# Optimization experiments

Measured on AMD Instinct MI355X. Metric: run time of the kernel, lower is better.

Reference implementation:

```python
import jax, jax.numpy as jnp
import numpy as np

D_MODEL = 1024
D_INNER = 2048   # expand * d_model
D_STATE = 16
D_CONV = 4
DT_RANK = 64     # ceil(d_model / 16)
BATCH = 4
SEQLEN = 2048


def _dw_causal_conv(x, w, b):
    # x: (B, d, L); w: (d, 1, K) depthwise; causal left pad K-1 -> output length L
    y = jax.lax.conv_general_dilated(
        x, w, window_strides=(1,), padding=[(D_CONV - 1, 0)],
        dimension_numbers=("NCH", "OIH", "NCH"), feature_group_count=x.shape[1])
    return y + b[None, :, None]


def _ssm_pass(x_conv, z, A_log, x_proj_w, dt_proj_w, dt_proj_b, D):
    # x_conv, z: (B, d, L)
    Bsz, d, L = x_conv.shape
    u = jax.nn.silu(x_conv)                                   # (B, d, L)
    x_dbl = jnp.einsum("bdl,rd->blr", u, x_proj_w)            # (B, L, dt_rank+2N)
    dt = x_dbl[..., :DT_RANK]
    Bm = x_dbl[..., DT_RANK:DT_RANK + D_STATE]                # (B, L, N)
    Cm = x_dbl[..., DT_RANK + D_STATE:]                       # (B, L, N)
    delta = jax.nn.softplus(jnp.einsum("blr,dr->bld", dt, dt_proj_w) + dt_proj_b)  # (B, L, d)
    A = -jnp.exp(A_log)                                       # (d, N)

    # time-major inputs for scan
    delta_t = jnp.transpose(delta, (1, 0, 2))                 # (L, B, d)
    u_t = jnp.transpose(u, (2, 0, 1))                         # (L, B, d)
    Bm_t = jnp.transpose(Bm, (1, 0, 2))                       # (L, B, N)
    Cm_t = jnp.transpose(Cm, (1, 0, 2))                       # (L, B, N)

    def step(h, inp):
        d_s, B_s, C_s, u_s = inp                              # (B,d) (B,N) (B,N) (B,d)
        dA = jnp.exp(d_s[:, :, None] * A)                     # (B, d, N)
        h = dA * h + (d_s * u_s)[:, :, None] * B_s[:, None, :]
        y = jnp.einsum("bdn,bn->bd", h, C_s)
        return h, y

    h0 = jnp.zeros((Bsz, d, D_STATE), dtype=u.dtype)
    _, ys = jax.lax.scan(step, h0, (delta_t, Bm_t, Cm_t, u_t))  # ys: (L, B, d)
    y = jnp.transpose(ys, (1, 2, 0)) + D[None, :, None] * u     # (B, d, L)
    return y * jax.nn.silu(z)


def setup_inputs() -> dict:
    key = jax.random.key(0)
    ks = jax.random.split(key, 16)
    s = 0.02
    hidden_states = jax.random.normal(ks[0], (BATCH, SEQLEN, D_MODEL), jnp.float32)
    in_proj_w = jax.random.normal(ks[1], (2 * D_INNER, D_MODEL), jnp.float32) * s
    conv_w_f = jax.random.normal(ks[2], (D_INNER, 1, D_CONV), jnp.float32) * 0.2
    conv_b_f = jax.random.normal(ks[3], (D_INNER,), jnp.float32) * 0.1
    conv_w_b = jax.random.normal(ks[4], (D_INNER, 1, D_CONV), jnp.float32) * 0.2
    conv_b_b = jax.random.normal(ks[5], (D_INNER,), jnp.float32) * 0.1
    x_proj_w_f = jax.random.normal(ks[6], (DT_RANK + 2 * D_STATE, D_INNER), jnp.float32) * s
    dt_proj_w_f = jax.random.uniform(ks[7], (D_INNER, DT_RANK), jnp.float32, -DT_RANK**-0.5, DT_RANK**-0.5)
    x_proj_w_b = jax.random.normal(ks[8], (DT_RANK + 2 * D_STATE, D_INNER), jnp.float32) * s
    dt_proj_w_b = jax.random.uniform(ks[9], (D_INNER, DT_RANK), jnp.float32, -DT_RANK**-0.5, DT_RANK**-0.5)
    # dt bias init: inverse-softplus of dt sampled log-uniform in [1e-3, 1e-1]
    dt = jnp.exp(jax.random.uniform(ks[10], (D_INNER,)) * (np.log(0.1) - np.log(0.001)) + np.log(0.001))
    dt = jnp.clip(dt, 1e-4, None)
    inv_dt = dt + jnp.log(-jnp.expm1(-dt))
    dt_proj_b_f = inv_dt
    dt_proj_b_b = inv_dt
    A_log = jnp.log(jnp.broadcast_to(jnp.arange(1, D_STATE + 1, dtype=jnp.float32), (D_INNER, D_STATE)))
    out_proj_w = jax.random.normal(ks[11], (D_MODEL, D_INNER), jnp.float32) * s
    return {
        "hidden_states": hidden_states, "in_proj_w": in_proj_w,
        "conv_w_f": conv_w_f, "conv_b_f": conv_b_f, "conv_w_b": conv_w_b, "conv_b_b": conv_b_b,
        "x_proj_w_f": x_proj_w_f, "dt_proj_w_f": dt_proj_w_f, "dt_proj_b_f": dt_proj_b_f,
        "x_proj_w_b": x_proj_w_b, "dt_proj_w_b": dt_proj_w_b, "dt_proj_b_b": dt_proj_b_b,
        "A_log_f": A_log, "A_log_b": A_log,
        "D_f": jnp.ones((D_INNER,), jnp.float32), "D_b": jnp.ones((D_INNER,), jnp.float32),
        "out_proj_w": out_proj_w,
    }


def reference(hidden_states, in_proj_w, conv_w_f, conv_b_f, conv_w_b, conv_b_b,
              x_proj_w_f, dt_proj_w_f, dt_proj_b_f, x_proj_w_b, dt_proj_w_b, dt_proj_b_b,
              A_log_f, A_log_b, D_f, D_b, out_proj_w):
    L = hidden_states.shape[1]
    xz = jnp.einsum("bld,ed->bel", hidden_states, in_proj_w)  # (B, 2*d_inner, L)
    x, z = xz[:, :D_INNER], xz[:, D_INNER:]

    # forward direction
    x_conv_f = _dw_causal_conv(x, conv_w_f, conv_b_f)[..., :L]
    y_f = _ssm_pass(x_conv_f, z, A_log_f, x_proj_w_f, dt_proj_w_f, dt_proj_b_f, D_f)

    # backward direction
    x_b, z_b = x[..., ::-1], z[..., ::-1]
    x_conv_b = _dw_causal_conv(x_b, conv_w_b, conv_b_b)[..., :L]
    y_b = _ssm_pass(x_conv_b, z_b, A_log_b, x_proj_w_b, dt_proj_w_b, dt_proj_b_b, D_b)[..., ::-1]

    y = (y_f + y_b) / 2.0                                     # if_divide_out=True
    out = jnp.einsum("bdl,ed->ble", y, out_proj_w)            # (B, L, d_model)
    return out
```

## Files before the change

kernel.cpp:

```cpp
#include <hip/hip_runtime.h>


#define Bsz  4
#define LSEQ 2048
#define DM   1024
#define DI   2048
#define DS   16
#define MROWS (Bsz * LSEQ)
#define NCH  32
#define CLEN 64

typedef unsigned short u16b;
typedef __attribute__((ext_vector_type(8))) short short8;
typedef __attribute__((ext_vector_type(4))) float f32x4;
typedef __attribute__((address_space(3))) unsigned int lds_u32;
typedef const __attribute__((address_space(1))) unsigned int glb_u32;

__device__ __forceinline__ float b2f(u16b u) {
  union { unsigned int i; float f; } x; x.i = ((unsigned int)u) << 16; return x.f;
}
__device__ __forceinline__ u16b f2b(float f) {
  union { float f; unsigned int i; } x; x.f = f;
  unsigned int r = x.i + 0x7FFFu + ((x.i >> 16) & 1u);
  return (u16b)(r >> 16);
}
__device__ __forceinline__ u16b f2b_cvt(float f) {
  unsigned int r;
  asm("v_cvt_pk_bf16_f32 %0, %1, %1" : "=v"(r) : "v"(f));
  return (u16b)r;
}
__device__ __forceinline__ float fast_rcp(float x) {
  return __builtin_amdgcn_rcpf(x);
}
__device__ __forceinline__ float softplus_fast(float v) {
  float e = __expf(-fabsf(v));
  return fmaxf(v, 0.f) + __logf(1.f + e);
}
__device__ __forceinline__ void pow_ladder(float q, float* dA) {
  float q2 = q * q, q3 = q2 * q, q4 = q2 * q2;
  float q5 = q4 * q, q6 = q4 * q2, q7 = q4 * q3, q8 = q4 * q4;
  dA[0] = q;  dA[1] = q2;  dA[2] = q3;  dA[3] = q4;
  dA[4] = q5; dA[5] = q6;  dA[6] = q7;  dA[7] = q8;
  dA[8] = q8 * q;  dA[9] = q8 * q2;  dA[10] = q8 * q3;  dA[11] = q8 * q4;
  dA[12] = q8 * q5; dA[13] = q8 * q6; dA[14] = q8 * q7; dA[15] = q8 * q8;
}

__device__ __forceinline__ int xcd_swz(int id, int nwg) {
  int c = nwg >> 3;
  return (id & 7) * c + (id >> 3);
}

__device__ __forceinline__ void stage_tile(const u16b* gbase, int ld,
                                           u16b* lds, int wave, int lane) {
#pragma unroll
  for (int t = 0; t < 4; ++t) {
    int rb = wave * 32 + t * 8;
    int r = rb + (lane >> 3);
    int cb = (lane & 7) ^ (r & 7);
    const u16b* g = gbase + (size_t)r * ld + cb * 8;
    __builtin_amdgcn_global_load_lds((glb_u32*)g, (lds_u32*)(lds + rb * 64),
                                     16, 0, 0);
  }
}

__device__ __forceinline__ void stage_half(const u16b* gbase, int ld,
                                           u16b* ldsbase, int tid) {
#pragma unroll
  for (int i2 = 0; i2 < 2; ++i2) {
    int rg = (tid >> 6) * 2 + i2;
    int row = rg * 8 + ((tid >> 3) & 7);
    int cb = (tid & 7) ^ (row & 7);
    const u16b* g = gbase + (size_t)row * ld + cb * 8;
    __builtin_amdgcn_global_load_lds((glb_u32*)g,
                                     (lds_u32*)(ldsbase + rg * 8 * 64), 16, 0, 0);
  }
}

__global__ void sniff_kernel(const unsigned int* __restrict__ p,
                             int* __restrict__ flag) {
  unsigned int w = p[threadIdx.x];
  int e = (w >> 7) & 0xFF;
  unsigned long long m = __ballot(e >= 110 && e <= 135);
  if (threadIdx.x == 0) *flag = (__popcll(m) >= 32) ? 1 : 0;
}

struct ConvTab { const void* s[17]; u16b* d[17]; };
__global__ __launch_bounds__(256) void convert_all_kernel(
    ConvTab t, const int* __restrict__ flag) {
  const int pref[18] = {0, 4096, 6144, 7168, 7172, 7173, 7177, 7178, 7274,
                        7338, 7339, 7435, 7499, 7500, 7516, 7532, 7533, 7534};
  int bx = blockIdx.x;
  int seg = 0;
#pragma unroll
  for (int i = 0; i < 17; ++i)
    if (bx >= pref[i + 1]) seg = i + 1;
  int idx = (bx - pref[seg]) * 2048 + threadIdx.x * 8;
  u16b* dst = t.d[seg];
  if (*flag) {
    *(uint4*)(dst + idx) = *(const uint4*)((const u16b*)t.s[seg] + idx);
  } else {
    const float* s = (const float*)t.s[seg];
    float4 a = *(const float4*)(s + idx);
    float4 b = *(const float4*)(s + idx + 4);
    u16b o[8] = {f2b(a.x), f2b(a.y), f2b(a.z), f2b(a.w),
                 f2b(b.x), f2b(b.y), f2b(b.z), f2b(b.w)};
    *(uint4*)(dst + idx) = *(uint4*)o;
  }
}

__global__ __launch_bounds__(512, 2) void gemm8_kernel(
    const u16b* __restrict__ A, const u16b* __restrict__ B,
    u16b* __restrict__ C, int M, int N, int K, int lda, int ldb, int ldc) {
  __shared__ u16b As[2][256 * 64];
  __shared__ u16b Bs[2][256 * 64];
  const int tid = threadIdx.x;
  const int nbx = gridDim.x;
  const int id = xcd_swz(blockIdx.y * nbx + blockIdx.x, nbx * gridDim.y);
  const int n0 = (id % nbx) * 256;
  const int m0 = (id / nbx) * 256;
  const int wave = tid >> 6, lane = tid & 63;
  const int wm = (wave >> 2) * 128, wn = (wave & 3) * 64;
  const int lr = lane & 15, lg = lane >> 4;

  const u16b* Ab = A + (size_t)m0 * lda;
  const u16b* Bb = B + (size_t)n0 * ldb;
  const int nt = K >> 6;

  f32x4 acc[8][4] = {};

  stage_half(Ab, lda, As[0], tid);
  stage_half(Ab + (size_t)128 * lda, lda, As[0] + 8192, tid);
  stage_half(Bb, ldb, Bs[0], tid);
  stage_half(Bb + (size_t)128 * ldb, ldb, Bs[0] + 8192, tid);
  asm volatile("s_waitcnt vmcnt(0)" ::: "memory");
  __builtin_amdgcn_s_barrier();

  for (int t = 0; t < nt; ++t) {
    const int cur = t & 1;
    const u16b* Ac = As[cur];
    const u16b* Bc = Bs[cur];
    u16b* An = As[cur ^ 1];
    u16b* Bn = Bs[cur ^ 1];
    const int k1 = (t + 1) << 6;
    const bool more = (t + 1 < nt);
#pragma unroll
    for (int q = 0; q < 4; ++q) {
      short8 afr[4][2], bfr[2][2];
#pragma unroll
      for (int i = 0; i < 4; ++i) {
        int r = wm + (q >> 1) * 64 + i * 16 + lr;
#pragma unroll
        for (int kx = 0; kx < 2; ++kx)
          afr[i][kx] = *(const short8*)&Ac[r * 64 + ((kx * 4 + lg) ^ (r & 7)) * 8];
      }
#pragma unroll
      for (int j = 0; j < 2; ++j) {
        int r = wn + (q & 1) * 32 + j * 16 + lr;
#pragma unroll
        for (int kx = 0; kx < 2; ++kx)
          bfr[j][kx] = *(const short8*)&Bc[r * 64 + ((kx * 4 + lg) ^ (r & 7)) * 8];
      }
      if (more) {
        if (q == 0) stage_half(Ab + k1, lda, An, tid);
        else if (q == 1) stage_half(Ab + (size_t)128 * lda + k1, lda, An + 8192, tid);
        else if (q == 2) stage_half(Bb + k1, ldb, Bn, tid);
        else stage_half(Bb + (size_t)128 * ldb + k1, ldb, Bn + 8192, tid);
      }
      __builtin_amdgcn_s_barrier();
      asm volatile("s_waitcnt lgkmcnt(0)" ::: "memory");
      __builtin_amdgcn_sched_barrier(0);
      __builtin_amdgcn_s_setprio(1);
#pragma unroll
      for (int kx = 0; kx < 2; ++kx)
#pragma unroll
        for (int i = 0; i < 4; ++i)
#pragma unroll
          for (int j = 0; j < 2; ++j)
            acc[(q >> 1) * 4 + i][(q & 1) * 2 + j] =
                __builtin_amdgcn_mfma_f32_16x16x32_bf16(
                    afr[i][kx], bfr[j][kx],
                    acc[(q >> 1) * 4 + i][(q & 1) * 2 + j], 0, 0, 0);
      __builtin_amdgcn_s_setprio(0);
      __builtin_amdgcn_sched_barrier(0);
      __builtin_amdgcn_s_barrier();
    }
    asm volatile("s_waitcnt vmcnt(0)" ::: "memory");
    __builtin_amdgcn_s_barrier();
  }

#pragma unroll
  for (int i = 0; i < 8; ++i) {
    int rbase = m0 + wm + i * 16 + lg * 4;
#pragma unroll
    for (int j = 0; j < 4; ++j) {
      int col = n0 + wn + j * 16 + lr;
      if (col < N) {
#pragma unroll
        for (int e = 0; e < 4; ++e)
          C[(size_t)(rbase + e) * ldc + col] = f2b(acc[i][j][e]);
      }
    }
  }
}

#define BM 128
#define BN 128
#define BK 64

template<int EPI>
__global__ __launch_bounds__(256) void gemm_kernel(
    const u16b* __restrict__ A, const u16b* __restrict__ B, void* __restrict__ Cptr,
    const int* __restrict__ flag, int M, int N, int K, int lda, int ldb, int ldc) {
  __shared__ u16b As[BM * BK];
  __shared__ u16b Bs[BN * BK];
  const int tid = threadIdx.x;
  const int nbx = gridDim.x;
  const int id = xcd_swz(blockIdx.y * nbx + blockIdx.x, nbx * gridDim.y);
  const int n0 = (id % nbx) * BN;
  const int m0 = (id / nbx) * BM;
  const int wave = tid >> 6, lane = tid & 63;
  const int wm = (wave >> 1) * 64, wn = (wave & 1) * 64;
  const int lr = lane & 15, lg = lane >> 4;
  u16b* C = (u16b*)Cptr;
  float* Cf = (float*)Cptr;
  const int fl = (EPI == 3) ? flag[0] : 1;

  f32x4 acc[4][4] = {};

  for (int k0 = 0; k0 < K; k0 += BK) {
    stage_tile(A + (size_t)m0 * lda + k0, lda, As, wave, lane);
    stage_tile(B + (size_t)n0 * ldb + k0, ldb, Bs, wave, lane);
    __syncthreads();
#pragma unroll
    for (int kk = 0; kk < BK; kk += 32) {
      short8 afr[4], bfr[4];
#pragma unroll
      for (int i = 0; i < 4; ++i) {
        int r = wm + i * 16 + lr;
        afr[i] = *(const short8*)&As[r * 64 + (((kk >> 3) + lg) ^ (r & 7)) * 8];
      }
#pragma unroll
      for (int j = 0; j < 4; ++j) {
        int r = wn + j * 16 + lr;
        bfr[j] = *(const short8*)&Bs[r * 64 + (((kk >> 3) + lg) ^ (r & 7)) * 8];
      }
#pragma unroll
      for (int i = 0; i < 4; ++i)
#pragma unroll
        for (int j = 0; j < 4; ++j)
          acc[i][j] = __builtin_amdgcn_mfma_f32_16x16x32_bf16(
              afr[i], bfr[j], acc[i][j], 0, 0, 0);
    }
    __syncthreads();
  }

#pragma unroll
  for (int i = 0; i < 4; ++i) {
    int rbase = m0 + wm + i * 16 + lg * 4;
#pragma unroll
    for (int j = 0; j < 4; ++j) {
      int col = n0 + wn + j * 16 + lr;
      if (col < N) {
#pragma unroll
        for (int e = 0; e < 4; ++e) {
          float v = acc[i][j][e];
          size_t ci = (size_t)(rbase + e) * ldc + col;
          if (EPI == 3) {
            if (fl) C[ci] = f2b(v); else Cf[ci] = v;
          } else {
            C[ci] = f2b(v);
          }
        }
      }
    }
  }
}

template<int EPI>
__global__ __launch_bounds__(256) void gemm2_kernel(
    const u16b* __restrict__ A, const u16b* __restrict__ B1,
    const u16b* __restrict__ B2, u16b* __restrict__ C1, u16b* __restrict__ C2,
    const u16b* __restrict__ bias1, const u16b* __restrict__ bias2,
    float* __restrict__ aux1, float* __restrict__ aux2,
    int Mhalf, int N, int K, int lda, int ldb, int ldc1, int ldc2) {
  __shared__ u16b As[BM * BK];
  __shared__ u16b Bs[BN * BK];
  const int tid = threadIdx.x;
  const int nbx = gridDim.x;
  const int id = xcd_swz(blockIdx.y * nbx + blockIdx.x, nbx * gridDim.y);
  const int n0 = (id % nbx) * BN;
  const int m0 = (id / nbx) * BM;
  const int hi = (m0 >= Mhalf);
  const u16b* B = hi ? B2 : B1;
  u16b* C = hi ? C2 : C1;
  const u16b* bias = hi ? bias2 : bias1;
  float* aux = hi ? aux2 : aux1;
  const int ldc = hi ? ldc2 : ldc1;
  const int mloc = m0 - (hi ? Mhalf : 0);
  const int wave = tid >> 6, lane = tid & 63;
  const int wm = (wave >> 1) * 64, wn = (wave & 1) * 64;
  const int lr = lane & 15, lg = lane >> 4;

  f32x4 acc[4][4] = {};

  for (int k0 = 0; k0 < K; k0 += BK) {
    stage_tile(A + (size_t)m0 * lda + k0, lda, As, wave, lane);
    stage_tile(B + (size_t)n0 * ldb + k0, ldb, Bs, wave, lane);
    __syncthreads();
#pragma unroll
    for (int kk = 0; kk < BK; kk += 32) {
      short8 afr[4], bfr[4];
#pragma unroll
      for (int i = 0; i < 4; ++i) {
        int r = wm + i * 16 + lr;
        afr[i] = *(const short8*)&As[r * 64 + (((kk >> 3) + lg) ^ (r & 7)) * 8];
      }
#pragma unroll
      for (int j = 0; j < 4; ++j) {
        int r = wn + j * 16 + lr;
        bfr[j] = *(const short8*)&Bs[r * 64 + (((kk >> 3) + lg) ^ (r & 7)) * 8];
      }
#pragma unroll
      for (int i = 0; i < 4; ++i)
#pragma unroll
        for (int j = 0; j < 4; ++j)
          acc[i][j] = __builtin_amdgcn_mfma_f32_16x16x32_bf16(
              afr[i], bfr[j], acc[i][j], 0, 0, 0);
    }
    __syncthreads();
  }

#pragma unroll
  for (int i = 0; i < 4; ++i) {
    int rbase = mloc + wm + i * 16 + lg * 4;
#pragma unroll
    for (int j = 0; j < 4; ++j) {
      int col = n0 + wn + j * 16 + lr;
      if (col < N) {
        float bv = (EPI == 1) ? b2f(bias[col]) : 0.f;
#pragma unroll
        for (int e = 0; e < 4; ++e) {
          float v = acc[i][j][e];
          if (EPI == 1) v = softplus_fast(v + bv);
          C[(size_t)(rbase + e) * ldc + col] = f2b(v);
          if (EPI == 2 && col >= 64)
            aux[(size_t)(rbase + e) * 32 + (col - 64)] = v;
        }
      }
    }
  }
}

__global__ __launch_bounds__(256) void gemm2s_kernel(
    const u16b* __restrict__ A, const u16b* __restrict__ B1,
    const u16b* __restrict__ B2, float* __restrict__ P,
    int Mhalf, int Ksplit, int lda, int ldb) {
  __shared__ u16b As[BM * BK];
  __shared__ u16b Bs[BN * BK];
  const int tid = threadIdx.x;
  const int ks = blockIdx.x;
  const int m0 = blockIdx.y * BM;
  const int hi = (m0 >= Mhalf);
  const u16b* B = hi ? B2 : B1;
  const int wave = tid >> 6, lane = tid & 63;
  const int wm = (wave >> 1) * 64, wn = (wave & 1) * 64;
  const int lr = lane & 15, lg = lane >> 4;

  f32x4 acc[4][4] = {};

  const int kbeg = ks * Ksplit;
  for (int k0 = kbeg; k0 < kbeg + Ksplit; k0 += BK) {
    stage_tile(A + (size_t)m0 * lda + k0, lda, As, wave, lane);
    stage_tile(B + k0, ldb, Bs, wave, lane);
    __syncthreads();
#pragma unroll
    for (int kk = 0; kk < BK; kk += 32) {
      short8 afr[4], bfr[4];
#pragma unroll
      for (int i = 0; i < 4; ++i) {
        int r = wm + i * 16 + lr;
        afr[i] = *(const short8*)&As[r * 64 + (((kk >> 3) + lg) ^ (r & 7)) * 8];
      }
#pragma unroll
      for (int j = 0; j < 4; ++j) {
        int r = wn + j * 16 + lr;
        bfr[j] = *(const short8*)&Bs[r * 64 + (((kk >> 3) + lg) ^ (r & 7)) * 8];
      }
#pragma unroll
      for (int i = 0; i < 4; ++i)
#pragma unroll
        for (int j = 0; j < 4; ++j)
          acc[i][j] = __builtin_amdgcn_mfma_f32_16x16x32_bf16(
              afr[i], bfr[j], acc[i][j], 0, 0, 0);
    }
    __syncthreads();
  }

  float* Pk = P + (size_t)ks * ((size_t)2 * Mhalf) * 128;
#pragma unroll
  for (int i = 0; i < 4; ++i) {
    int rg = m0 + wm + i * 16 + lg * 4;
#pragma unroll
    for (int j = 0; j < 4; ++j) {
      int col = wn + j * 16 + lr;
#pragma unroll
      for (int e = 0; e < 4; ++e)
        Pk[(size_t)(rg + e) * 128 + col] = acc[i][j][e];
    }
  }
}

__global__ __launch_bounds__(256) void xdbl_reduce_kernel(
    const float* __restrict__ P, u16b* __restrict__ xdf,
    u16b* __restrict__ xdb, float* __restrict__ bcf,
    float* __restrict__ bcb) {
  int e = blockIdx.x * 256 + threadIdx.x;
  int col = e & 127;
  int m = e >> 7;
  if (col >= 96) return;
  float v = P[(size_t)e] + P[(size_t)e + (size_t)16384 * 128];
  int hi = (m >= MROWS);
  int mloc = m - (hi ? MROWS : 0);
  u16b* C = hi ? xdb : xdf;
  C[(size_t)mloc * 96 + col] = f2b(v);
  if (col >= 64) {
    float* aux = hi ? bcb : bcf;
    aux[(size_t)mloc * 32 + (col - 64)] = v;
  }
}

__global__ __launch_bounds__(256) void conv_kernel(
    const u16b* __restrict__ xz, const u16b* __restrict__ cwf,
    const u16b* __restrict__ cbf, const u16b* __restrict__ cwb,
    const u16b* __restrict__ cbb, u16b* __restrict__ u_f,
    u16b* __restrict__ u_b) {
  int gid = blockIdx.x * 256 + threadIdx.x;
  int d = gid & (DI - 1);
  int m = gid >> 11;
  int b = m >> 11;
  int l = m & (LSEQ - 1);
  const u16b* xcol = xz + ((size_t)b * LSEQ) * (2 * DI) + d;
  float xv[7];
#pragma unroll
  for (int t = 0; t < 7; ++t) {
    int ll = l + t - 3;
    xv[t] = (ll >= 0 && ll < LSEQ) ? b2f(xcol[(size_t)ll * (2 * DI)]) : 0.f;
  }
  float af = b2f(cbf[d]);
#pragma unroll
  for (int k = 0; k < 4; ++k) af = fmaf(b2f(cwf[d * 4 + k]), xv[k], af);
  float ab = b2f(cbb[d]);
#pragma unroll
  for (int j = 0; j < 4; ++j) ab = fmaf(b2f(cwb[d * 4 + 3 - j]), xv[3 + j], ab);
  float sf = af * fast_rcp(1.f + __expf(-af));
  float sb = ab * fast_rcp(1.f + __expf(-ab));
  u_f[(size_t)m * DI + d] = f2b(sf);
  u_b[((size_t)b * LSEQ + (LSEQ - 1 - l)) * DI + d] = f2b(sb);
}

__device__ __forceinline__ bool detect_intA(const u16b* alog, int d, float* An2) {
  bool fast = true;
#pragma unroll
  for (int n = 0; n < DS; ++n) {
    float a = __expf(b2f(alog[d * DS + n]));
    An2[n] = -a * 1.44269504088896f;
    fast = fast && (fabsf(a - (float)(n + 1)) < 0.02f * (float)(n + 1));
  }
  return fast;
}

#define CHUNK_BODY_FAST() do {                                        \
    float du = cd * cu; s += cd;                                      \
    float dA[DS]; pow_ladder(__expf(-cd), dA);                        \
    _Pragma("unroll") for (int n = 0; n < DS; ++n)                    \
      h[n] = fmaf(dA[n], h[n], du * bl[n]);                           \
    bl += 32;                                                         \
  } while (0)

#define CHUNK_BODY_SLOW() do {                                        \
    float du = cd * cu; s += cd;                                      \
    _Pragma("unroll") for (int n = 0; n < DS; ++n) {                  \
      float dA = exp2f(cd * An2[n]);                                  \
      h[n] = fmaf(dA, h[n], du * bl[n]);                              \
    }                                                                 \
    bl += 32;                                                         \
  } while (0)

__global__ __launch_bounds__(256) void scan_chunk_kernel(
    const u16b* __restrict__ xz, const u16b* __restrict__ u_f,
    const u16b* __restrict__ u_b, const u16b* __restrict__ dltb,
    const float* __restrict__ bc_f, const float* __restrict__ bc_b,
    const u16b* __restrict__ alog_f, const u16b* __restrict__ alog_b,
    float* __restrict__ hstate, float* __restrict__ sdelta) {
  int bx = blockIdx.x;
  int dblk = bx & 7;
  int chunk = (bx >> 3) & 31;
  if (chunk == NCH - 1) return;
  int b = (bx >> 8) & 3;
  int dir = bx >> 10;
  int d = dblk * 256 + threadIdx.x;

  const u16b* uptr = dir ? u_b : u_f;
  const u16b* dlt = dir ? dltb : xz;
  const int ldd = dir ? DI : 2 * DI;
  const float* bcp = dir ? bc_b : bc_f;
  const u16b* alog = dir ? alog_b : alog_f;

  const size_t mb = (size_t)b * LSEQ + (size_t)chunk * CLEN;
  const float* bl = bcp + mb * 32;
  float An2[DS];
  bool fastA = detect_intA(alog, d, An2);

  float h[DS];
#pragma unroll
  for (int n = 0; n < DS; ++n) h[n] = 0.f;
  float s = 0.f;
  unsigned od = (unsigned)mb * (unsigned)ldd + (unsigned)d;
  unsigned ou = (unsigned)mb * DI + (unsigned)d;
  float nd = b2f(dlt[od]);
  float nu = b2f(uptr[ou]);
  float cd, cu;
  if (fastA) {
#pragma unroll 4
    for (int l = 0; l < CLEN - 1; ++l) {
      cd = nd; cu = nu;
      od += ldd; ou += DI;
      nd = b2f(dlt[od]); nu = b2f(uptr[ou]);
      CHUNK_BODY_FAST();
    }
    cd = nd; cu = nu;
    CHUNK_BODY_FAST();
  } else {
#pragma unroll 4
    for (int l = 0; l < CLEN - 1; ++l) {
      cd = nd; cu = nu;
      od += ldd; ou += DI;
      nd = b2f(dlt[od]); nu = b2f(uptr[ou]);
      CHUNK_BODY_SLOW();
    }
    cd = nd; cu = nu;
    CHUNK_BODY_SLOW();
  }
  size_t slot = (size_t)((dir * 4 + b) * 32 + chunk) * 2048 + d;
  float* hp = hstate + slot * 16;
#pragma unroll
  for (int i = 0; i < 4; ++i)
    ((f32x4*)hp)[i] = *(f32x4*)&h[i * 4];
  sdelta[slot] = s;
}

__global__ __launch_bounds__(256) void scan_carry_kernel(
    const u16b* __restrict__ alog_f, const u16b* __restrict__ alog_b,
    float* __restrict__ hstate, const float* __restrict__ sdelta) {
  int gid = blockIdx.x * 256 + threadIdx.x;
  int n = gid & (DS - 1);
  int d = (gid >> 4) & (DI - 1);
  int b = (gid >> 15) & 3;
  int dir = gid >> 17;
  const u16b* alog = dir ? alog_b : alog_f;
  float An2 = -__expf(b2f(alog[d * DS + n])) * 1.44269504088896f;
  float h = 0.f;
  size_t base = (size_t)((dir * 4 + b) * 32) * 2048 + d;
  for (int c = 0; c < NCH; ++c) {
    size_t slot = base + (size_t)c * 2048;
    float* hp = hstate + slot * 16 + n;
    float hw = h;
    if (c + 1 < NCH) {
      float hl = *hp;
      float sdv = sdelta[slot];
      float P = exp2f(An2 * sdv);
      h = fmaf(P, h, hl);
    }
    *hp = hw;
  }
}

#define APPLY_BODY_FAST() do {                                        \
    float du = cd * cu;                                               \
    float dA[DS]; pow_ladder(__expf(-cd), dA);                        \
    float y0 = 0.f, y1 = 0.f;                                         \
    _Pragma("unroll") for (int n = 0; n < DS; n += 2) {               \
      h[n] = fmaf(dA[n], h[n], du * bl[n]);                           \
      y0 = fmaf(h[n], bl[16 + n], y0);                                \
      h[n + 1] = fmaf(dA[n + 1], h[n + 1], du * bl[n + 1]);           \
      y1 = fmaf(h[n + 1], bl[17 + n], y1);                            \
    }                                                                 \
    float sz = cz * fast_rcp(1.f + __expf(-cz));                      \
    float out = (y0 + y1 + Dd * cu) * sz;                             \
    uptr[oo] = f2b_cvt(out); oo += DI; bl += 32;                      \
  } while (0)

#define APPLY_BODY_SLOW() do {                                        \
    float du = cd * cu;                                               \
    float y = 0.f;                                                    \
    _Pragma("unroll") for (int n = 0; n < DS; ++n) {                  \
      float dA = exp2f(cd * An2[n]);                                  \
      h[n] = fmaf(dA, h[n], du * bl[n]);                              \
      y = fmaf(h[n], bl[16 + n], y);                                  \
    }                                                                 \
    float sz = cz * fast_rcp(1.f + __expf(-cz));                      \
    float out = (y + Dd * cu) * sz;                                   \
    uptr[oo] = f2b_cvt(out); oo += DI; bl += 32;                      \
  } while (0)

__global__ __launch_bounds__(256) void scan_apply_kernel(
    const u16b* __restrict__ xz, u16b* __restrict__ u_f,
    u16b* __restrict__ u_b, const u16b* __restrict__ dltb,
    const float* __restrict__ bc_f, const float* __restrict__ bc_b,
    const u16b* __restrict__ alog_f, const u16b* __restrict__ alog_b,
    const u16b* __restrict__ dv_f, const u16b* __restrict__ dv_b,
    const float* __restrict__ hstate) {
  int bx = blockIdx.x;
  int dblk = bx & 7;
  int chunk = (bx >> 3) & 31;
  int b = (bx >> 8) & 3;
  int dir = bx >> 10;
  int d = dblk * 256 + threadIdx.x;

  u16b* uptr = dir ? u_b : u_f;
  const u16b* dlt = dir ? dltb : xz;
  const int ldd = dir ? DI : 2 * DI;
  const float* bcp = dir ? bc_b : bc_f;
  const u16b* alog = dir ? alog_b : alog_f;
  const u16b* dv = dir ? dv_b : dv_f;

  const size_t mb0 = (size_t)b * LSEQ;
  const size_t mb = mb0 + (size_t)chunk * CLEN;
  const float* bl = bcp + mb * 32;
  float An2[DS];
  bool fastA = detect_intA(alog, d, An2);
  float Dd = b2f(dv[d]);
  float h[DS];
  {
    size_t slot = (size_t)((dir * 4 + b) * 32 + chunk) * 2048 + d;
    const float* hp = hstate + slot * 16;
#pragma unroll
    for (int i = 0; i < 4; ++i)
      *(f32x4*)&h[i * 4] = ((const f32x4*)hp)[i];
  }

  size_t zs0 = dir ? (mb0 + (LSEQ - 1 - (size_t)chunk * CLEN)) : mb;
  const int zst = dir ? -(2 * DI) : (2 * DI);
  unsigned od = (unsigned)mb * (unsigned)ldd + (unsigned)d;
  unsigned ou = (unsigned)mb * DI + (unsigned)d;
  unsigned oo = ou;
  int oz = (int)zs0 * (2 * DI) + DI + d;
  float nd = b2f(dlt[od]);
  float nu = b2f(uptr[ou]);
  float nz = b2f(xz[oz]);
  float cd, cu, cz;
  if (fastA) {
#pragma unroll 4
    for (int l = 0; l < CLEN - 1; ++l) {
      cd = nd; cu = nu; cz = nz;
      od += ldd; ou += DI; oz += zst;
      nd = b2f(dlt[od]); nu = b2f(uptr[ou]); nz = b2f(xz[oz]);
      APPLY_BODY_FAST();
    }
    cd = nd; cu = nu; cz = nz;
    APPLY_BODY_FAST();
  } else {
#pragma unroll 4
    for (int l = 0; l < CLEN - 1; ++l) {
      cd = nd; cu = nu; cz = nz;
      od += ldd; ou += DI; oz += zst;
      nd = b2f(dlt[od]); nu = b2f(uptr[ou]); nz = b2f(xz[oz]);
      APPLY_BODY_SLOW();
    }
    cd = nd; cu = nu; cz = nz;
    APPLY_BODY_SLOW();
  }
}

__global__ __launch_bounds__(256) void combine_kernel(
    const u16b* __restrict__ yf, const u16b* __restrict__ yb_rev,
    u16b* __restrict__ yc) {
  size_t i = ((size_t)blockIdx.x * 256 + threadIdx.x) * 8;
  size_t m = i >> 11;
  size_t dcol = i & (DI - 1);
  size_t mr = m ^ (LSEQ - 1);
  uint4 a = *(const uint4*)(yf + m * DI + dcol);
  uint4 b = *(const uint4*)(yb_rev + mr * DI + dcol);
  const u16b* ap = (const u16b*)&a;
  const u16b* bp = (const u16b*)&b;
  uint4 o;
  u16b* op = (u16b*)&o;
#pragma unroll
  for (int j = 0; j < 8; ++j) op[j] = f2b(0.5f * (b2f(ap[j]) + b2f(bp[j])));
  *(uint4*)(yc + i) = o;
}

extern "C" void kernel_launch(void* const* d_in, const int* in_sizes, int n_in,
                              void* d_out, int out_size, void* d_ws,
                              size_t ws_size, hipStream_t stream) {
  char* ws = (char*)d_ws;
  u16b* xz    = (u16b*)(ws);
  u16b* u_f   = (u16b*)(ws + 67108864);
  u16b* u_b   = (u16b*)(ws + 100663296);
  u16b* arena = (u16b*)(ws + 134217728);
  u16b* xdf   = (u16b*)(ws + 167772160);
  u16b* xdb   = (u16b*)(ws + 169345024);
  float* bcf  = (float*)(ws + 170917888);
  float* bcb  = (float*)(ws + 171966464);
  u16b* opw_c  = (u16b*)(ws + 173015040);
  u16b* xpwf_c = (u16b*)(ws + 177209344);
  u16b* xpwb_c = (u16b*)(ws + 177602560);
  u16b* dpwf_c = (u16b*)(ws + 177995776);
  u16b* dpwb_c = (u16b*)(ws + 178257920);
  u16b* cwf_c  = (u16b*)(ws + 178520064);
  u16b* cwb_c  = (u16b*)(ws + 178536448);
  u16b* cbf_c  = (u16b*)(ws + 178552832);
  u16b* cbb_c  = (u16b*)(ws + 178556928);
  u16b* dpbf_c = (u16b*)(ws + 178561024);
  u16b* dpbb_c = (u16b*)(ws + 178565120);
  u16b* alf_c  = (u16b*)(ws + 178569216);
  u16b* alb_c  = (u16b*)(ws + 178634752);
  u16b* dvf_c  = (u16b*)(ws + 178700288);
  u16b* dvb_c  = (u16b*)(ws + 178704384);
  int*  flag   = (int*)(ws + 178708480);
  float* hstate = (float*)(ws + 178712576);
  float* sdelta = (float*)(ws + 212267008);

  u16b* hs_c  = arena;
  u16b* inw_c = arena + 8388608;
  float* Pbuf = (float*)arena;
  u16b* dltb  = arena;
  u16b* y_c   = arena;

  dim3 blk(256);
  sniff_kernel<<<dim3(1), dim3(64), 0, stream>>>((const unsigned int*)d_in[0], flag);
  ConvTab ct = {{d_in[0], d_in[1], d_in[16],
                 d_in[2], d_in[3], d_in[4], d_in[5], d_in[6], d_in[7], d_in[8],
                 d_in[9], d_in[10], d_in[11], d_in[12], d_in[13], d_in[14],
                 d_in[15]},
                {hs_c, inw_c, opw_c,
                 cwf_c, cbf_c, cwb_c, cbb_c, xpwf_c, dpwf_c, dpbf_c, xpwb_c,
                 dpwb_c, dpbb_c, alf_c, alb_c, dvf_c, dvb_c}};
  convert_all_kernel<<<dim3(7534), blk, 0, stream>>>(ct, flag);

  gemm8_kernel<<<dim3(16, 32), dim3(512), 0, stream>>>(hs_c, inw_c, xz,
      MROWS, 2 * DI, DM, DM, DM, 2 * DI);
  conv_kernel<<<dim3(65536), blk, 0, stream>>>(xz, cwf_c, cbf_c, cwb_c, cbb_c,
                                               u_f, u_b);
  gemm2s_kernel<<<dim3(2, 128), blk, 0, stream>>>(u_f, xpwf_c, xpwb_c, Pbuf,
      MROWS, 1024, DI, DI);
  xdbl_reduce_kernel<<<dim3(8192), blk, 0, stream>>>(Pbuf, xdf, xdb, bcf, bcb);
  gemm2_kernel<1><<<dim3(16, 128), blk, 0, stream>>>(xdf, dpwf_c, dpwb_c,
      xz, dltb, dpbf_c, dpbb_c, nullptr, nullptr, MROWS, DI, 64, 96, 64,
      2 * DI, DI);
  scan_chunk_kernel<<<dim3(2048), blk, 0, stream>>>(xz, u_f, u_b, dltb, bcf,
      bcb, alf_c, alb_c, hstate, sdelta);
  scan_carry_kernel<<<dim3(1024), blk, 0, stream>>>(alf_c, alb_c, hstate, sdelta);
  scan_apply_kernel<<<dim3(2048), blk, 0, stream>>>(xz, u_f, u_b, dltb, bcf,
      bcb, alf_c, alb_c, dvf_c, dvb_c, hstate);
  combine_kernel<<<dim3(8192), blk, 0, stream>>>(u_f, u_b, y_c);
  gemm_kernel<3><<<dim3(8, 64), blk, 0, stream>>>(y_c, opw_c, d_out, flag,
      MROWS, DM, DI, DI, DI, DM);
}
```

Baseline: 540.8 us.

## Restructure GEMM K-loop into 32-wide slices with counted vmcnt pipelining

```diff
diff --git a/kernel.cpp b/kernel.cpp
--- a/kernel.cpp
+++ b/kernel.cpp
@@ -63,16 +63,17 @@
   }
 }
 
-__device__ __forceinline__ void stage_half(const u16b* gbase, int ld,
-                                           u16b* ldsbase, int tid) {
-#pragma unroll
-  for (int i2 = 0; i2 < 2; ++i2) {
-    int rg = (tid >> 6) * 2 + i2;
-    int row = rg * 8 + ((tid >> 3) & 7);
-    int cb = (tid & 7) ^ (row & 7);
-    const u16b* g = gbase + (size_t)row * ld + cb * 8;
-    __builtin_amdgcn_global_load_lds((glb_u32*)g,
-                                     (lds_u32*)(ldsbase + rg * 8 * 64), 16, 0, 0);
+__device__ __forceinline__ void stage_slice(const u16b* gbase, int ld,
+                                            u16b* dst, int tid) {
+#pragma unroll
+  for (int i = 0; i < 2; ++i) {
+    int c = (tid >> 6) * 2 + i;
+    int l = tid & 63;
+    int row = c * 16 + 2 * (l >> 3) + ((l >> 2) & 1);
+    int gb = (l & 3) ^ ((l >> 3) & 3);
+    const u16b* g = gbase + (size_t)row * ld + gb * 8;
+    __builtin_amdgcn_global_load_lds((glb_u32*)g, (lds_u32*)(dst + c * 512),
+                                     16, 0, 0);
   }
 }
 
@@ -111,8 +112,8 @@
 __global__ __launch_bounds__(512, 2) void gemm8_kernel(
     const u16b* __restrict__ A, const u16b* __restrict__ B,
     u16b* __restrict__ C, int M, int N, int K, int lda, int ldb, int ldc) {
-  __shared__ u16b As[2][256 * 64];
-  __shared__ u16b Bs[2][256 * 64];
+  __shared__ u16b As[2][2 * 8192];
+  __shared__ u16b Bs[2][2 * 8192];
   const int tid = threadIdx.x;
   const int nbx = gridDim.x;
   const int id = xcd_swz(blockIdx.y * nbx + blockIdx.x, nbx * gridDim.y);
@@ -128,64 +129,53 @@
 
   f32x4 acc[8][4] = {};
 
-  stage_half(Ab, lda, As[0], tid);
-  stage_half(Ab + (size_t)128 * lda, lda, As[0] + 8192, tid);
-  stage_half(Bb, ldb, Bs[0], tid);
-  stage_half(Bb + (size_t)128 * ldb, ldb, Bs[0] + 8192, tid);
-  asm volatile("s_waitcnt vmcnt(0)" ::: "memory");
-  __builtin_amdgcn_s_barrier();
+  stage_slice(Ab, lda, As[0], tid);
+  stage_slice(Bb, ldb, Bs[0], tid);
+  stage_slice(Ab + 32, lda, As[0] + 8192, tid);
+  stage_slice(Bb + 32, ldb, Bs[0] + 8192, tid);
 
   for (int t = 0; t < nt; ++t) {
     const int cur = t & 1;
-    const u16b* Ac = As[cur];
-    const u16b* Bc = Bs[cur];
-    u16b* An = As[cur ^ 1];
-    u16b* Bn = Bs[cur ^ 1];
-    const int k1 = (t + 1) << 6;
     const bool more = (t + 1 < nt);
 #pragma unroll
-    for (int q = 0; q < 4; ++q) {
-      short8 afr[4][2], bfr[2][2];
-#pragma unroll
-      for (int i = 0; i < 4; ++i) {
-        int r = wm + (q >> 1) * 64 + i * 16 + lr;
-#pragma unroll
-        for (int kx = 0; kx < 2; ++kx)
-          afr[i][kx] = *(const short8*)&Ac[r * 64 + ((kx * 4 + lg) ^ (r & 7)) * 8];
-      }
-#pragma unroll
-      for (int j = 0; j < 2; ++j) {
-        int r = wn + (q & 1) * 32 + j * 16 + lr;
-#pragma unroll
-        for (int kx = 0; kx < 2; ++kx)
-          bfr[j][kx] = *(const short8*)&Bc[r * 64 + ((kx * 4 + lg) ^ (r & 7)) * 8];
-      }
+    for (int p = 0; p < 2; ++p) {
       if (more) {
-        if (q == 0) stage_half(Ab + k1, lda, An, tid);
-        else if (q == 1) stage_half(Ab + (size_t)128 * lda + k1, lda, An + 8192, tid);
-        else if (q == 2) stage_half(Bb + k1, ldb, Bn, tid);
-        else stage_half(Bb + (size_t)128 * ldb + k1, ldb, Bn + 8192, tid);
+        const int k1 = ((t + 1) << 6) + p * 32;
+        stage_slice(Ab + k1, lda, As[cur ^ 1] + p * 8192, tid);
+        stage_slice(Bb + k1, ldb, Bs[cur ^ 1] + p * 8192, tid);
+        asm volatile("s_waitcnt vmcnt(8)" ::: "memory");
+      } else {
+        if (p == 0) asm volatile("s_waitcnt vmcnt(4)" ::: "memory");
+        else        asm volatile("s_waitcnt vmcnt(0)" ::: "memory");
       }
       __builtin_amdgcn_s_barrier();
+      const u16b* Ac = As[cur] + p * 8192;
+      const u16b* Bc = Bs[cur] + p * 8192;
+      short8 afr[8], bfr[4];
+#pragma unroll
+      for (int i = 0; i < 8; ++i) {
+        int R = wm + i * 16 + lr;
+        afr[i] = *(const short8*)&Ac[(R >> 1) * 64 + (R & 1) * 32 +
+                                     ((lg ^ ((R >> 1) & 3)) * 8)];
+      }
+#pragma unroll
+      for (int j = 0; j < 4; ++j) {
+        int R = wn + j * 16 + lr;
+        bfr[j] = *(const short8*)&Bc[(R >> 1) * 64 + (R & 1) * 32 +
+                                     ((lg ^ ((R >> 1) & 3)) * 8)];
+      }
       asm volatile("s_waitcnt lgkmcnt(0)" ::: "memory");
       __builtin_amdgcn_sched_barrier(0);
       __builtin_amdgcn_s_setprio(1);
 #pragma unroll
-      for (int kx = 0; kx < 2; ++kx)
-#pragma unroll
-        for (int i = 0; i < 4; ++i)
-#pragma unroll
-          for (int j = 0; j < 2; ++j)
-            acc[(q >> 1) * 4 + i][(q & 1) * 2 + j] =
-                __builtin_amdgcn_mfma_f32_16x16x32_bf16(
-                    afr[i][kx], bfr[j][kx],
-                    acc[(q >> 1) * 4 + i][(q & 1) * 2 + j], 0, 0, 0);
+      for (int i = 0; i < 8; ++i)
+#pragma unroll
+        for (int j = 0; j < 4; ++j)
+          acc[i][j] = __builtin_amdgcn_mfma_f32_16x16x32_bf16(
+              afr[i], bfr[j], acc[i][j], 0, 0, 0);
       __builtin_amdgcn_s_setprio(0);
       __builtin_amdgcn_sched_barrier(0);
-      __builtin_amdgcn_s_barrier();
-    }
-    asm volatile("s_waitcnt vmcnt(0)" ::: "memory");
-    __builtin_amdgcn_s_barrier();
+    }
   }
 
 #pragma unroll
```

Result: slower. 585.3 us (+8.2%).
